# Optimization experiments

Hardware: AMD Instinct MI355X
Metric: run time of the kernel (lower is better)

## Reference

```python
import jax, jax.numpy as jnp
import numpy as np

N_HEAD = 16

def setup_inputs() -> dict:
    key = jax.random.key(0)
    ks = jax.random.split(key, 6)
    C = 1024
    B, T, Tp = 8, 1024, 64
    s = 0.02
    return {
        "x": jax.random.normal(ks[0], (B, T, C), jnp.float32),
        "prefix_embd": jax.random.normal(ks[1], (B, Tp, C), jnp.float32),
        "w_attn": jax.random.normal(ks[2], (C, 3 * C), jnp.float32) * s,
        "b_attn": jnp.zeros((3 * C,), jnp.float32),
        "w_prefix": jax.random.normal(ks[3], (C, 3 * C), jnp.float32) * s,
        "b_prefix": jnp.zeros((3 * C,), jnp.float32),
        "w_proj": jax.random.normal(ks[4], (C, C), jnp.float32) * s,
        "b_proj": jnp.zeros((C,), jnp.float32),
    }

def _heads(t, H):
    B, T, C = t.shape
    return t.reshape(B, T, H, C // H).transpose(0, 2, 1, 3)  # (B,H,T,d)

def reference(x, prefix_embd, w_attn, b_attn, w_prefix, b_prefix, w_proj, b_proj):
    B, T, C = x.shape
    H = N_HEAD
    d = C // H
    Tp = prefix_embd.shape[1]
    scale = 1.0 / jnp.sqrt(jnp.asarray(d, x.dtype))

    qkv = x @ w_attn + b_attn
    q, k, v = (_heads(t, H) for t in jnp.split(qkv, 3, axis=2))  # (B,H,T,d)

    pqkv = prefix_embd @ w_prefix + b_prefix
    _, k_p, v_p = (_heads(t, H) for t in jnp.split(pqkv, 3, axis=2))  # (B,H,Tp,d)

    causal = jnp.tril(jnp.ones((T, T), bool))  # bias buffer slice
    neg_inf = jnp.asarray(float("-inf"), x.dtype)

    att = jnp.einsum("bhqd,bhkd->bhqk", q, k) * scale
    att = jnp.where(causal[None, None], att, neg_inf)
    att = jax.nn.softmax(att, axis=-1)

    att_p = jnp.einsum("bhqd,bhkd->bhqk", q, k_p) * scale
    att_p = jnp.where(causal[:, :Tp][None, None], att_p, neg_inf)
    att_p = jax.nn.softmax(att_p, axis=-1)

    y = jnp.einsum("bhqk,bhkd->bhqd", att_p, v_p) + jnp.einsum("bhqk,bhkd->bhqd", att, v)
    y = y.transpose(0, 2, 1, 3).reshape(B, T, C)
    return y @ w_proj + b_proj
```

## Files before the change

### kernel.cpp

```cpp
#include <hip/hip_runtime.h>
#include <hip/hip_bf16.h>
#include <cstdint>
#include <cstddef>

typedef __bf16 bf16_t;
typedef bf16_t bf16x8 __attribute__((ext_vector_type(8)));
typedef bf16_t bf16x4 __attribute__((ext_vector_type(4)));
typedef float f32x4 __attribute__((ext_vector_type(4)));

#define NB 8
#define NT 1024
#define NC 1024
#define NH 16
#define ND 64
#define NTP 64

__global__ __launch_bounds__(256) void k_transpose_cast(const float* __restrict__ src,
                                                        bf16_t* __restrict__ dst,
                                                        int K, int N) {
    __shared__ float tile[32][33];
    int nt = blockIdx.x, kt = blockIdx.y;
    int tx = threadIdx.x & 31;
    int ty = threadIdx.x >> 5;
#pragma unroll
    for (int i = 0; i < 4; i++) {
        int r = ty + i * 8;
        tile[r][tx] = src[(size_t)(kt * 32 + r) * N + nt * 32 + tx];
    }
    __syncthreads();
#pragma unroll
    for (int i = 0; i < 4; i++) {
        int r = ty + i * 8;
        dst[(size_t)(nt * 32 + r) * K + kt * 32 + tx] = (bf16_t)tile[tx][r];
    }
}

template <bool AF32, int OMODE, int TSH>
__global__ __launch_bounds__(256) void k_gemm_f(const void* __restrict__ A,
                                                const bf16_t* __restrict__ BT,
                                                const float* __restrict__ bias,
                                                void* __restrict__ Cout,
                                                bf16_t* __restrict__ Vout,
                                                int M, int N, int K) {
    __shared__ bf16_t As[128 * 72];
    __shared__ bf16_t Bs[128 * 72];
    const int tid = threadIdx.x;
    const int lane = tid & 63;
    const int wave = tid >> 6;
    const int quad = lane >> 4;
    const int l15 = lane & 15;
    const int wm = (wave >> 1) * 64;
    const int wn = (wave & 1) * 64;
    const size_t rowA0 = (size_t)blockIdx.y * 128;
    const size_t colB0 = (size_t)blockIdx.x * 128;

    const f32x4 fz = {0.f, 0.f, 0.f, 0.f};
    f32x4 acc[4][4];
#pragma unroll
    for (int i = 0; i < 4; i++)
#pragma unroll
        for (int j = 0; j < 4; j++) acc[i][j] = fz;

    for (int k0 = 0; k0 < K; k0 += 64) {
        __syncthreads();
#pragma unroll
        for (int i = 0; i < 4; i++) {
            int c = tid + i * 256;
            int r = c >> 3;
            int kc = (c & 7) * 8;
            if (AF32) {
                const float* Af = (const float*)A + (rowA0 + r) * (size_t)K + k0 + kc;
                float4 a0 = *(const float4*)Af;
                float4 a1 = *(const float4*)(Af + 4);
                bf16x8 av;
                av[0] = (bf16_t)a0.x; av[1] = (bf16_t)a0.y;
                av[2] = (bf16_t)a0.z; av[3] = (bf16_t)a0.w;
                av[4] = (bf16_t)a1.x; av[5] = (bf16_t)a1.y;
                av[6] = (bf16_t)a1.z; av[7] = (bf16_t)a1.w;
                *(bf16x8*)(&As[r * 72 + kc]) = av;
            } else {
                uint4 av = *(const uint4*)((const bf16_t*)A + (rowA0 + r) * (size_t)K + k0 + kc);
                *(uint4*)(&As[r * 72 + kc]) = av;
            }
            uint4 bv = *(const uint4*)(BT + (colB0 + r) * (size_t)K + k0 + kc);
            *(uint4*)(&Bs[r * 72 + kc]) = bv;
        }
        __syncthreads();
#pragma unroll
        for (int kk = 0; kk < 2; kk++) {
            bf16x8 af[4], bfr[4];
#pragma unroll
            for (int i = 0; i < 4; i++)
                af[i] = *(const bf16x8*)(&As[(wm + i * 16 + l15) * 72 + kk * 32 + quad * 8]);
#pragma unroll
            for (int j = 0; j < 4; j++)
                bfr[j] = *(const bf16x8*)(&Bs[(wn + j * 16 + l15) * 72 + kk * 32 + quad * 8]);
#pragma unroll
            for (int i = 0; i < 4; i++)
#pragma unroll
                for (int j = 0; j < 4; j++)
                    acc[i][j] = __builtin_amdgcn_mfma_f32_16x16x32_bf16(af[i], bfr[j], acc[i][j], 0, 0, 0);
        }
    }
    const bool vpath = (OMODE == 2) && (colB0 >= (size_t)(2 * NC));
#pragma unroll
    for (int i = 0; i < 4; i++) {
        size_t row = rowA0 + wm + i * 16 + quad * 4;
#pragma unroll
        for (int j = 0; j < 4; j++) {
            int col = (int)colB0 + wn + j * 16 + l15;
            float bv = bias[col];
            if (vpath) {
                int hh = (col - 2 * NC) >> 6;
                int dd = col & 63;
                int bb = (int)(row >> TSH);
                int tt = (int)row & ((1 << TSH) - 1);
                size_t addr = ((size_t)(bb * NH + hh) * (1 << (TSH - 6)) + (tt >> 6)) * 4096
                              + (size_t)dd * 64 + (tt & 63);
                bf16x4 vv;
#pragma unroll
                for (int r = 0; r < 4; r++) vv[r] = (bf16_t)(acc[i][j][r] + bv);
                *(bf16x4*)(Vout + addr) = vv;
            } else {
#pragma unroll
                for (int r = 0; r < 4; r++) {
                    float v = acc[i][j][r] + bv;
                    if (OMODE == 1)
                        ((float*)Cout)[(row + r) * (size_t)N + col] = v;
                    else
                        ((bf16_t*)Cout)[(row + r) * (size_t)N + col] = (bf16_t)v;
                }
            }
        }
    }
}


#define LOADREGS(KB, VB)                                                  \
    rk0 = *(const uint4*)((KB) + (size_t)srow * 3072 + scol);             \
    rk1 = *(const uint4*)((KB) + (size_t)(srow + 32) * 3072 + scol);      \
    rv0 = *(const uint4*)((VB) + (size_t)tid * 8);                        \
    rv1 = *(const uint4*)((VB) + (size_t)(tid + 256) * 8);

#define STAGE(KS, VS)                                     \
    *(uint4*)(&(KS)[srow * 72 + scol]) = rk0;             \
    *(uint4*)(&(KS)[(srow + 32) * 72 + scol]) = rk1;      \
    *(uint4*)(&(VS)[srow * 72 + scol]) = rv0;             \
    *(uint4*)(&(VS)[(srow + 32) * 72 + scol]) = rv1;

#define QK(KS, Sj, j)                                                                  \
    Sj = __builtin_amdgcn_mfma_f32_16x16x32_bf16(                                      \
        aq0, *(const bf16x8*)(&(KS)[((j) * 16 + l15) * 72 + quad * 8]), Sj, 0, 0, 0);  \
    Sj = __builtin_amdgcn_mfma_f32_16x16x32_bf16(                                      \
        aq1, *(const bf16x8*)(&(KS)[((j) * 16 + l15) * 72 + 32 + quad * 8]), Sj, 0, 0, 0);

#define EXPJ(Sj, j, DIAG, LACC)                                         \
    {                                                                   \
        const int n_ = (j) * 16 + l15;                                  \
        _Pragma("unroll") for (int r_ = 0; r_ < 4; r_++) {              \
            float p_ = __expf(Sj[r_] * scale);                          \
            if ((DIAG) && n_ > wave * 16 + quad * 4 + r_) p_ = 0.f;     \
            Sj[r_] = p_;                                                \
            LACC[r_] += p_;                                             \
        }                                                               \
    }

#define PSTORE(Sj, j)                                                   \
    _Pragma("unroll") for (int r_ = 0; r_ < 4; r_++)                    \
        P[(quad * 4 + r_) * 72 + (j) * 16 + l15] = (bf16_t)Sj[r_];

#define PV(VS, Oj, j)                                                                  \
    Oj = __builtin_amdgcn_mfma_f32_16x16x32_bf16(                                      \
        ap0, *(const bf16x8*)(&(VS)[((j) * 16 + l15) * 72 + quad * 8]), Oj, 0, 0, 0);  \
    Oj = __builtin_amdgcn_mfma_f32_16x16x32_bf16(                                      \
        ap1, *(const bf16x8*)(&(VS)[((j) * 16 + l15) * 72 + 32 + quad * 8]), Oj, 0, 0, 0);

#define PROC(KS, VS, DIAG, LACC, O0, O1, O2, O3)                        \
    {                                                                   \
        f32x4 S0 = fz, S1 = fz, S2 = fz, S3 = fz;                       \
        QK(KS, S0, 0) QK(KS, S1, 1) QK(KS, S2, 2) QK(KS, S3, 3)         \
        EXPJ(S0, 0, DIAG, LACC) EXPJ(S1, 1, DIAG, LACC)                 \
        EXPJ(S2, 2, DIAG, LACC) EXPJ(S3, 3, DIAG, LACC)                 \
        PSTORE(S0, 0) PSTORE(S1, 1) PSTORE(S2, 2) PSTORE(S3, 3)         \
        __builtin_amdgcn_s_waitcnt(0xc07f);             \
        __builtin_amdgcn_wave_barrier();                                \
        bf16x8 ap0 = *(const bf16x8*)(&P[l15 * 72 + quad * 8]);         \
        bf16x8 ap1 = *(const bf16x8*)(&P[l15 * 72 + 32 + quad * 8]);    \
        PV(VS, O0, 0) PV(VS, O1, 1) PV(VS, O2, 2) PV(VS, O3, 3)         \
    }

#define STORE_O(Oj, Pj, j)                                                            \
    _Pragma("unroll") for (int r_ = 0; r_ < 4; r_++) {                                \
        float v_ = Oj[r_] * lmv[r_] + Pj[r_] * lpv[r_];                               \
        y[(qrow0 + quad * 4 + r_) * NC + h * 64 + (j) * 16 + l15] = (bf16_t)v_;       \
    }

__global__ __launch_bounds__(256, 2) void k_attn8(const bf16_t* __restrict__ qkv,
                                                  const bf16_t* __restrict__ pqkv,
                                                  const bf16_t* __restrict__ vp,
                                                  const bf16_t* __restrict__ pvp,
                                                  bf16_t* __restrict__ y) {
    const int qt = (NT / 64 - 1) - blockIdx.x;
    const int h = blockIdx.y;
    const int b = blockIdx.z;

    __shared__ bf16_t Ks0[64 * 72], Ks1[64 * 72];
    __shared__ bf16_t Vs0[64 * 72], Vs1[64 * 72];
    __shared__ bf16_t Ps[4][16 * 72];

    const int tid = threadIdx.x;
    const int lane = tid & 63;
    const int wave = tid >> 6;
    const int quad = lane >> 4;
    const int l15 = lane & 15;
    const int srow = tid >> 3;
    const int scol = (tid & 7) * 8;
    const float scale = 0.125f;

    const size_t qrow0 = (size_t)b * NT + (size_t)qt * 64 + wave * 16;
    bf16_t* P = Ps[wave];

    const bf16_t* Kmain = qkv + (size_t)(b * NT) * 3072 + NC + h * 64;
    const bf16_t* Vmain = vp + (size_t)(b * NH + h) * 16 * (64 * 64);

    bf16x8 aq0 = *(const bf16x8*)(qkv + (qrow0 + l15) * 3072 + h * 64 + quad * 8);
    bf16x8 aq1 = *(const bf16x8*)(qkv + (qrow0 + l15) * 3072 + h * 64 + 32 + quad * 8);

    const f32x4 fz = {0.f, 0.f, 0.f, 0.f};
    f32x4 Om0 = fz, Om1 = fz, Om2 = fz, Om3 = fz;
    f32x4 Op0 = fz, Op1 = fz, Op2 = fz, Op3 = fz;
    f32x4 Lm = fz, Lp = fz;
    uint4 rk0, rk1, rv0, rv1;

    LOADREGS(pqkv + (size_t)(b * NTP) * 3072 + NC + h * 64,
             pvp + (size_t)(b * NH + h) * (NTP * 64))
    STAGE(Ks0, Vs0)
    LOADREGS(Kmain, Vmain)
    __syncthreads();
    PROC(Ks0, Vs0, qt == 0, Lp, Op0, Op1, Op2, Op3)
    STAGE(Ks1, Vs1)
    if (qt >= 1) { LOADREGS(Kmain + (size_t)64 * 3072, Vmain + 64 * 64) }

    for (int t = 0; t <= qt; t++) {
        __syncthreads();
        bf16_t* KSc = (t & 1) ? Ks0 : Ks1;
        bf16_t* VSc = (t & 1) ? Vs0 : Vs1;
        if (t < qt) {
            bf16_t* KSn = (t & 1) ? Ks1 : Ks0;
            bf16_t* VSn = (t & 1) ? Vs1 : Vs0;
            STAGE(KSn, VSn)
        }
        if (t + 1 < qt) {
            LOADREGS(Kmain + ((size_t)(t + 2) * 64) * 3072, Vmain + (size_t)(t + 2) * (64 * 64))
        }
        PROC(KSc, VSc, t == qt, Lm, Om0, Om1, Om2, Om3)
    }

    f32x4 lmv, lpv;
#pragma unroll
    for (int r = 0; r < 4; r++) {
        float vm = Lm[r], vpr = Lp[r];
#pragma unroll
        for (int off = 1; off < 16; off <<= 1) {
            vm += __shfl_xor(vm, off, 64);
            vpr += __shfl_xor(vpr, off, 64);
        }
        lmv[r] = 1.0f / vm;
        lpv[r] = 1.0f / vpr;
    }

    STORE_O(Om0, Op0, 0) STORE_O(Om1, Op1, 1) STORE_O(Om2, Op2, 2) STORE_O(Om3, Op3, 3)
}

extern "C" void kernel_launch(void* const* d_in, const int* in_sizes, int n_in,
                              void* d_out, int out_size, void* d_ws, size_t ws_size,
                              hipStream_t stream) {
    (void)in_sizes; (void)n_in; (void)out_size; (void)ws_size;
    const float* x        = (const float*)d_in[0];
    const float* prefix   = (const float*)d_in[1];
    const float* w_attn   = (const float*)d_in[2];
    const float* b_attn   = (const float*)d_in[3];
    const float* w_prefix = (const float*)d_in[4];
    const float* b_prefix = (const float*)d_in[5];
    const float* w_proj   = (const float*)d_in[6];
    const float* b_proj   = (const float*)d_in[7];
    float* out = (float*)d_out;

    char* p = (char*)d_ws;
    auto carve = [&](size_t bytes) {
        char* q = p;
        p += (bytes + 255) & ~(size_t)255;
        return q;
    };
    bf16_t* vp   = (bf16_t*)carve((size_t)NB * NT * NC * 2);
    bf16_t* pvp  = (bf16_t*)carve((size_t)NB * NTP * NC * 2);
    bf16_t* wTa  = (bf16_t*)carve((size_t)3 * NC * NC * 2);
    bf16_t* wTp  = (bf16_t*)carve((size_t)3 * NC * NC * 2);
    bf16_t* wTpr = (bf16_t*)carve((size_t)NC * NC * 2);
    bf16_t* qkv  = (bf16_t*)carve((size_t)NB * NT * 3 * NC * 2);
    bf16_t* pqkv = (bf16_t*)carve((size_t)NB * NTP * 3 * NC * 2);
    bf16_t* yb   = (bf16_t*)carve((size_t)NB * NT * NC * 2);

    k_transpose_cast<<<dim3(3 * NC / 32, NC / 32), 256, 0, stream>>>(w_attn, wTa, NC, 3 * NC);
    k_transpose_cast<<<dim3(3 * NC / 32, NC / 32), 256, 0, stream>>>(w_prefix, wTp, NC, 3 * NC);
    k_transpose_cast<<<dim3(NC / 32, NC / 32), 256, 0, stream>>>(w_proj, wTpr, NC, NC);
    k_gemm_f<true, 2, 10><<<dim3(3 * NC / 128, NB * NT / 128), 256, 0, stream>>>(
        x, wTa, b_attn, qkv, vp, NB * NT, 3 * NC, NC);
    k_gemm_f<true, 2, 6><<<dim3(3 * NC / 128, NB * NTP / 128), 256, 0, stream>>>(
        prefix, wTp, b_prefix, pqkv, pvp, NB * NTP, 3 * NC, NC);
    k_attn8<<<dim3(NT / 64, NH, NB), 256, 0, stream>>>(qkv, pqkv, vp, pvp, yb);
    k_gemm_f<false, 1, 6><<<dim3(NC / 128, NB * NT / 128), 256, 0, stream>>>(
        yb, wTpr, b_proj, out, nullptr, NB * NT, NC, NC);
}
```

Baseline: 358.4 us.

## Pre-cast activations, merge weight transposes, store V in qkv slot, add setprio

```diff
diff --git a/kernel.cpp b/kernel.cpp
--- a/kernel.cpp
+++ b/kernel.cpp
@@ -15,10 +15,37 @@
 #define ND 64
 #define NTP 64
 
-__global__ __launch_bounds__(256) void k_transpose_cast(const float* __restrict__ src,
-                                                        bf16_t* __restrict__ dst,
-                                                        int K, int N) {
+__global__ __launch_bounds__(256) void k_cast2(const float* __restrict__ a, bf16_t* __restrict__ da,
+                                               int n4a,
+                                               const float* __restrict__ b2, bf16_t* __restrict__ db,
+                                               int n4b) {
+    int i = blockIdx.x * 256 + threadIdx.x;
+    if (i < n4a) {
+        float4 f = ((const float4*)a)[i];
+        bf16x4 o;
+        o[0] = (bf16_t)f.x; o[1] = (bf16_t)f.y; o[2] = (bf16_t)f.z; o[3] = (bf16_t)f.w;
+        ((bf16x4*)da)[i] = o;
+    } else {
+        int j = i - n4a;
+        if (j < n4b) {
+            float4 f = ((const float4*)b2)[j];
+            bf16x4 o;
+            o[0] = (bf16_t)f.x; o[1] = (bf16_t)f.y; o[2] = (bf16_t)f.z; o[3] = (bf16_t)f.w;
+            ((bf16x4*)db)[j] = o;
+        }
+    }
+}
+
+__global__ __launch_bounds__(256) void k_transpose3(const float* __restrict__ s0, bf16_t* __restrict__ d0,
+                                                    const float* __restrict__ s1, bf16_t* __restrict__ d1,
+                                                    const float* __restrict__ s2, bf16_t* __restrict__ d2) {
     __shared__ float tile[32][33];
+    const int z = blockIdx.z;
+    const float* src = (z == 0) ? s0 : (z == 1) ? s1 : s2;
+    bf16_t* dst = (z == 0) ? d0 : (z == 1) ? d1 : d2;
+    const int N = (z == 2) ? NC : 3 * NC;
+    const int K = NC;
+    if (z == 2 && blockIdx.x >= 32) return;
     int nt = blockIdx.x, kt = blockIdx.y;
     int tx = threadIdx.x & 31;
     int ty = threadIdx.x >> 5;
@@ -35,12 +62,11 @@
     }
 }
 
-template <bool AF32, int OMODE, int TSH>
-__global__ __launch_bounds__(256) void k_gemm_f(const void* __restrict__ A,
+template <int OMODE, int TSH>
+__global__ __launch_bounds__(256) void k_gemm_f(const bf16_t* __restrict__ A,
                                                 const bf16_t* __restrict__ BT,
                                                 const float* __restrict__ bias,
                                                 void* __restrict__ Cout,
-                                                bf16_t* __restrict__ Vout,
                                                 int M, int N, int K) {
     __shared__ bf16_t As[128 * 72];
     __shared__ bf16_t Bs[128 * 72];
@@ -68,20 +94,8 @@
             int c = tid + i * 256;
             int r = c >> 3;
             int kc = (c & 7) * 8;
-            if (AF32) {
-                const float* Af = (const float*)A + (rowA0 + r) * (size_t)K + k0 + kc;
-                float4 a0 = *(const float4*)Af;
-                float4 a1 = *(const float4*)(Af + 4);
-                bf16x8 av;
-                av[0] = (bf16_t)a0.x; av[1] = (bf16_t)a0.y;
-                av[2] = (bf16_t)a0.z; av[3] = (bf16_t)a0.w;
-                av[4] = (bf16_t)a1.x; av[5] = (bf16_t)a1.y;
-                av[6] = (bf16_t)a1.z; av[7] = (bf16_t)a1.w;
-                *(bf16x8*)(&As[r * 72 + kc]) = av;
-            } else {
-                uint4 av = *(const uint4*)((const bf16_t*)A + (rowA0 + r) * (size_t)K + k0 + kc);
-                *(uint4*)(&As[r * 72 + kc]) = av;
-            }
+            uint4 av = *(const uint4*)(A + (rowA0 + r) * (size_t)K + k0 + kc);
+            *(uint4*)(&As[r * 72 + kc]) = av;
             uint4 bv = *(const uint4*)(BT + (colB0 + r) * (size_t)K + k0 + kc);
             *(uint4*)(&Bs[r * 72 + kc]) = bv;
         }
@@ -115,12 +129,13 @@
                 int dd = col & 63;
                 int bb = (int)(row >> TSH);
                 int tt = (int)row & ((1 << TSH) - 1);
-                size_t addr = ((size_t)(bb * NH + hh) * (1 << (TSH - 6)) + (tt >> 6)) * 4096
-                              + (size_t)dd * 64 + (tt & 63);
+                int tileBase = (bb * NH + hh) * (1 << (TSH - 6)) + (tt >> 6);
+                size_t chunkrow = (size_t)tileBase * 4 + (dd >> 4);
+                size_t addr = chunkrow * (size_t)N + 2 * NC + (dd & 15) * 64 + (tt & 63);
                 bf16x4 vv;
 #pragma unroll
                 for (int r = 0; r < 4; r++) vv[r] = (bf16_t)(acc[i][j][r] + bv);
-                *(bf16x4*)(Vout + addr) = vv;
+                *(bf16x4*)((bf16_t*)Cout + addr) = vv;
             } else {
 #pragma unroll
                 for (int r = 0; r < 4; r++) {
@@ -136,11 +151,11 @@
 }
 
 
-#define LOADREGS(KB, VB)                                                  \
-    rk0 = *(const uint4*)((KB) + (size_t)srow * 3072 + scol);             \
-    rk1 = *(const uint4*)((KB) + (size_t)(srow + 32) * 3072 + scol);      \
-    rv0 = *(const uint4*)((VB) + (size_t)tid * 8);                        \
-    rv1 = *(const uint4*)((VB) + (size_t)(tid + 256) * 8);
+#define LOADREGS(KB, VCB)                                                            \
+    rk0 = *(const uint4*)((KB) + (size_t)srow * 3072 + scol);                        \
+    rk1 = *(const uint4*)((KB) + (size_t)(srow + 32) * 3072 + scol);                 \
+    rv0 = *(const uint4*)((VCB) + (size_t)(tid >> 7) * 3072 + (tid & 127) * 8);      \
+    rv1 = *(const uint4*)((VCB) + (size_t)((tid >> 7) + 2) * 3072 + (tid & 127) * 8);
 
 #define STAGE(KS, VS)                                     \
     *(uint4*)(&(KS)[srow * 72 + scol]) = rk0;             \
@@ -178,7 +193,9 @@
 #define PROC(KS, VS, DIAG, LACC, O0, O1, O2, O3)                        \
     {                                                                   \
         f32x4 S0 = fz, S1 = fz, S2 = fz, S3 = fz;                       \
+        __builtin_amdgcn_s_setprio(1);                                  \
         QK(KS, S0, 0) QK(KS, S1, 1) QK(KS, S2, 2) QK(KS, S3, 3)         \
+        __builtin_amdgcn_s_setprio(0);                                  \
         EXPJ(S0, 0, DIAG, LACC) EXPJ(S1, 1, DIAG, LACC)                 \
         EXPJ(S2, 2, DIAG, LACC) EXPJ(S3, 3, DIAG, LACC)                 \
         PSTORE(S0, 0) PSTORE(S1, 1) PSTORE(S2, 2) PSTORE(S3, 3)         \
@@ -186,7 +203,9 @@
         __builtin_amdgcn_wave_barrier();                                \
         bf16x8 ap0 = *(const bf16x8*)(&P[l15 * 72 + quad * 8]);         \
         bf16x8 ap1 = *(const bf16x8*)(&P[l15 * 72 + 32 + quad * 8]);    \
+        __builtin_amdgcn_s_setprio(1);                                  \
         PV(VS, O0, 0) PV(VS, O1, 1) PV(VS, O2, 2) PV(VS, O3, 3)         \
+        __builtin_amdgcn_s_setprio(0);                                  \
     }
 
 #define STORE_O(Oj, Pj, j)                                                            \
@@ -195,11 +214,9 @@
         y[(qrow0 + quad * 4 + r_) * NC + h * 64 + (j) * 16 + l15] = (bf16_t)v_;       \
     }
 
-__global__ __launch_bounds__(256, 2) void k_attn8(const bf16_t* __restrict__ qkv,
-                                                  const bf16_t* __restrict__ pqkv,
-                                                  const bf16_t* __restrict__ vp,
-                                                  const bf16_t* __restrict__ pvp,
-                                                  bf16_t* __restrict__ y) {
+__global__ __launch_bounds__(256, 2) void k_attn10(const bf16_t* __restrict__ qkv,
+                                                   const bf16_t* __restrict__ pqkv,
+                                                   bf16_t* __restrict__ y) {
     const int qt = (NT / 64 - 1) - blockIdx.x;
     const int h = blockIdx.y;
     const int b = blockIdx.z;
@@ -221,7 +238,8 @@
     bf16_t* P = Ps[wave];
 
     const bf16_t* Kmain = qkv + (size_t)(b * NT) * 3072 + NC + h * 64;
-    const bf16_t* Vmain = vp + (size_t)(b * NH + h) * 16 * (64 * 64);
+    const bf16_t* Vmain = qkv + (size_t)(b * NH + h) * 16 * 4 * 3072 + 2 * NC;
+    const bf16_t* Vpre  = pqkv + (size_t)(b * NH + h) * 4 * 3072 + 2 * NC;
 
     bf16x8 aq0 = *(const bf16x8*)(qkv + (qrow0 + l15) * 3072 + h * 64 + quad * 8);
     bf16x8 aq1 = *(const bf16x8*)(qkv + (qrow0 + l15) * 3072 + h * 64 + 32 + quad * 8);
@@ -232,14 +250,13 @@
     f32x4 Lm = fz, Lp = fz;
     uint4 rk0, rk1, rv0, rv1;
 
-    LOADREGS(pqkv + (size_t)(b * NTP) * 3072 + NC + h * 64,
-             pvp + (size_t)(b * NH + h) * (NTP * 64))
+    LOADREGS(pqkv + (size_t)(b * NTP) * 3072 + NC + h * 64, Vpre)
     STAGE(Ks0, Vs0)
     LOADREGS(Kmain, Vmain)
     __syncthreads();
     PROC(Ks0, Vs0, qt == 0, Lp, Op0, Op1, Op2, Op3)
     STAGE(Ks1, Vs1)
-    if (qt >= 1) { LOADREGS(Kmain + (size_t)64 * 3072, Vmain + 64 * 64) }
+    if (qt >= 1) { LOADREGS(Kmain + (size_t)64 * 3072, Vmain + 4 * 3072) }
 
     for (int t = 0; t <= qt; t++) {
         __syncthreads();
@@ -251,7 +268,7 @@
             STAGE(KSn, VSn)
         }
         if (t + 1 < qt) {
-            LOADREGS(Kmain + ((size_t)(t + 2) * 64) * 3072, Vmain + (size_t)(t + 2) * (64 * 64))
+            LOADREGS(Kmain + ((size_t)(t + 2) * 64) * 3072, Vmain + (size_t)(t + 2) * 4 * 3072)
         }
         PROC(KSc, VSc, t == qt, Lm, Om0, Om1, Om2, Om3)
     }
@@ -292,8 +309,8 @@
         p += (bytes + 255) & ~(size_t)255;
         return q;
     };
-    bf16_t* vp   = (bf16_t*)carve((size_t)NB * NT * NC * 2);
-    bf16_t* pvp  = (bf16_t*)carve((size_t)NB * NTP * NC * 2);
+    bf16_t* xb   = (bf16_t*)carve((size_t)NB * NT * NC * 2);
+    bf16_t* pb   = (bf16_t*)carve((size_t)NB * NTP * NC * 2);
     bf16_t* wTa  = (bf16_t*)carve((size_t)3 * NC * NC * 2);
     bf16_t* wTp  = (bf16_t*)carve((size_t)3 * NC * NC * 2);
     bf16_t* wTpr = (bf16_t*)carve((size_t)NC * NC * 2);
@@ -301,14 +318,15 @@
     bf16_t* pqkv = (bf16_t*)carve((size_t)NB * NTP * 3 * NC * 2);
     bf16_t* yb   = (bf16_t*)carve((size_t)NB * NT * NC * 2);
 
-    k_transpose_cast<<<dim3(3 * NC / 32, NC / 32), 256, 0, stream>>>(w_attn, wTa, NC, 3 * NC);
-    k_transpose_cast<<<dim3(3 * NC / 32, NC / 32), 256, 0, stream>>>(w_prefix, wTp, NC, 3 * NC);
-    k_transpose_cast<<<dim3(NC / 32, NC / 32), 256, 0, stream>>>(w_proj, wTpr, NC, NC);
-    k_gemm_f<true, 2, 10><<<dim3(3 * NC / 128, NB * NT / 128), 256, 0, stream>>>(
-        x, wTa, b_attn, qkv, vp, NB * NT, 3 * NC, NC);
-    k_gemm_f<true, 2, 6><<<dim3(3 * NC / 128, NB * NTP / 128), 256, 0, stream>>>(
-        prefix, wTp, b_prefix, pqkv, pvp, NB * NTP, 3 * NC, NC);
-    k_attn8<<<dim3(NT / 64, NH, NB), 256, 0, stream>>>(qkv, pqkv, vp, pvp, yb);
-    k_gemm_f<false, 1, 6><<<dim3(NC / 128, NB * NT / 128), 256, 0, stream>>>(
-        yb, wTpr, b_proj, out, nullptr, NB * NT, NC, NC);
-}
+    const int n4a = NB * NT * NC / 4, n4b = NB * NTP * NC / 4;
+    k_cast2<<<(n4a + n4b + 255) / 256, 256, 0, stream>>>(x, xb, n4a, prefix, pb, n4b);
+    k_transpose3<<<dim3(3 * NC / 32, NC / 32, 3), 256, 0, stream>>>(w_attn, wTa, w_prefix, wTp,
+                                                                    w_proj, wTpr);
+    k_gemm_f<2, 10><<<dim3(3 * NC / 128, NB * NT / 128), 256, 0, stream>>>(
+        xb, wTa, b_attn, qkv, NB * NT, 3 * NC, NC);
+    k_gemm_f<2, 6><<<dim3(3 * NC / 128, NB * NTP / 128), 256, 0, stream>>>(
+        pb, wTp, b_prefix, pqkv, NB * NTP, 3 * NC, NC);
+    k_attn10<<<dim3(NT / 64, NH, NB), 256, 0, stream>>>(qkv, pqkv, yb);
+    k_gemm_f<1, 6><<<dim3(NC / 128, NB * NT / 128), 256, 0, stream>>>(
+        yb, wTpr, b_proj, out, NB * NT, NC, NC);
+}
```

New measurement: 310.9 us. -13.3%, faster.
